# Performance work log

Measured on AMD Instinct MI355X. Metric: run time of the kernel, lower is better.

The kernel has to match this reference:

```python
import jax, jax.numpy as jnp
import numpy as np
from jax import lax

MAXW = 4  # spans cover j in [i, min(i+4, max_len)) -> widths 1..4


def setup_inputs() -> dict:
    key = jax.random.key(0)
    ks = jax.random.split(key, 8)
    B, L, H = 64, 512, 256
    Hd = H // 2  # dynamicLSTM hidden = kernel_num/2
    s = 0.05
    feats = jax.random.normal(ks[0], (B, L, H), dtype=jnp.float32)
    lens = jax.random.randint(ks[1], (B,), 1, L + 1)
    W_ih = jax.random.normal(ks[2], (4 * Hd, H), dtype=jnp.float32) * s
    W_hh = jax.random.normal(ks[3], (4 * Hd, Hd), dtype=jnp.float32) * s
    b_ih = jax.random.normal(ks[4], (4 * Hd,), dtype=jnp.float32) * s
    b_hh = jax.random.normal(ks[5], (4 * Hd,), dtype=jnp.float32) * s
    W_tri = jax.random.normal(ks[6], (2, Hd), dtype=jnp.float32) * s
    b_tri = jax.random.normal(ks[7], (2,), dtype=jnp.float32) * s
    return {"feats": feats, "W_ih": W_ih, "W_hh": W_hh, "b_ih": b_ih,
            "b_hh": b_hh, "W_tri": W_tri, "b_tri": b_tri, "lens": lens}


def _build_tag_graph(feats, W_ih, W_hh, b_ih, b_hh, W_tri, b_tri, lens):
    B, Lmax, H = feats.shape
    Hd = W_hh.shape[1]
    starts = jnp.arange(Lmax)
    idx = starts[:, None] + jnp.arange(MAXW)[None, :]              # (L, 4)
    in_range = idx < Lmax
    win = feats[:, jnp.minimum(idx, Lmax - 1)] * in_range[None, :, :, None]  # (B, L, 4, H)
    x = win.transpose(2, 0, 1, 3).reshape(MAXW, B * Lmax, H)       # steps-major

    def step(carry, xt):
        h, c = carry
        gates = xt @ W_ih.T + b_ih + h @ W_hh.T + b_hh
        i_, f_, g_, o_ = jnp.split(gates, 4, axis=-1)  # torch gate order i,f,g,o
        c = jax.nn.sigmoid(f_) * c + jax.nn.sigmoid(i_) * jnp.tanh(g_)
        h = jax.nn.sigmoid(o_) * jnp.tanh(c)
        return (h, c), h

    h0 = jnp.zeros((B * Lmax, Hd), feats.dtype)
    _, hs = lax.scan(step, (h0, h0), x)                            # (4, B*L, Hd)
    hs = hs.reshape(MAXW, B, Lmax, Hd).transpose(1, 2, 0, 3)       # (B, L, 4, Hd); [...,t,:] = hidden after t+1 steps

    # effective packed length per span: total = clip(lens - i, 0, w); pack uses max(total, 1)
    w = jnp.arange(1, MAXW + 1)                                    # span widths
    rem = lens[:, None] - starts[None, :]                          # (B, L)
    total = jnp.clip(rem[:, :, None], 0, w[None, None, :])         # (B, L, 4)
    Lsel = jnp.maximum(total, 1)
    row_mask = (total > 0).astype(feats.dtype)
    h_span = jnp.take_along_axis(hs, (Lsel - 1)[..., None], axis=2)  # (B, L, 4, Hd)

    emit = (h_span @ W_tri.T + b_tri) * row_mask[..., None]        # (B, L, 4, 2)
    # scatter emit[b, i, w-1] into span_scores[b, i, i+w-1]; drop spans past max_len
    valid_span = in_range  # j = i + (w-1) < Lmax
    emit = emit * valid_span[None, :, :, None]
    j_clamped = jnp.minimum(idx, Lmax - 1)
    span_scores = jnp.zeros((B, Lmax, Lmax, 2), feats.dtype)
    span_scores = span_scores.at[:, starts[:, None], j_clamped].add(emit)
    return span_scores


def reference(feats, W_ih, W_hh, b_ih, b_hh, W_tri, b_tri, lens):
    return _build_tag_graph(feats, W_ih, W_hh, b_ih, b_hh, W_tri, b_tri, lens)
```

## Files before the change

kernel.cpp:

```cpp
#include <hip/hip_runtime.h>
#include <cstddef>

#define NB 64
#define LL 512
#define HH 256
#define HD 128
#define NG 512
#define TI 16

typedef _Float16 half_t;
typedef _Float16 half8 __attribute__((ext_vector_type(8)));
typedef _Float16 half4 __attribute__((ext_vector_type(4)));
typedef float f32x4 __attribute__((ext_vector_type(4)));

#define MFMA16(a, b, c) __builtin_amdgcn_mfma_f32_16x16x32_f16((a), (b), (c), 0, 0, 0)

#define FP 264
#define XP 522
#define HFP 132
#define HBP 136

__device__ __forceinline__ float sigm(float x)  { return 1.0f / (1.0f + __expf(-x)); }
__device__ __forceinline__ float tanhf_(float x){ return 2.0f / (1.0f + __expf(-2.0f * x)) - 1.0f; }

__global__ void prep_weights(const float* __restrict__ Wih, const float* __restrict__ Whh,
                             const float* __restrict__ bih, const float* __restrict__ bhh,
                             half_t* __restrict__ WihH, half_t* __restrict__ WhhH,
                             float* __restrict__ bsum)
{
    const int idx = blockIdx.x * 256 + threadIdx.x;
    if (idx < NG * HH) WihH[idx] = (half_t)Wih[idx];
    if (idx < NG * HD) WhhH[idx] = (half_t)Whh[idx];
    if (idx < NG)      bsum[idx] = bih[idx] + bhh[idx];
}

__global__ __launch_bounds__(256, 2) void span_lstm_mfma(
    const float* __restrict__ feats, const half_t* __restrict__ WihH,
    const half_t* __restrict__ WhhH, const float* __restrict__ bsum,
    const float* __restrict__ W_tri, const float* __restrict__ b_tri,
    const int* __restrict__ lens, float* __restrict__ out)
{
    __shared__ __align__(16) half_t sFeatb[32 * FP];
    __shared__ __align__(16) float  sXG[20 * XP];
    __shared__ __align__(16) float  sHf[16 * HFP];
    __shared__ __align__(16) half_t sHb[16 * HBP];
    __shared__ float sEmit[2][32];

    const int tid = threadIdx.x;
    const int b  = blockIdx.x >> 5;
    const int i0 = (blockIdx.x & 31) * TI;
    const int lens_b = lens[b];

    for (int idx = tid; idx < 20 * 64; idx += 256) {
        const int p  = idx >> 6;
        const int k4 = (idx & 63) << 2;
        const int gp = i0 + p;
        float4 v = make_float4(0.f, 0.f, 0.f, 0.f);
        if (gp < LL) v = *(const float4*)(feats + ((size_t)b * LL + gp) * HH + k4);
        half4 hv = {(half_t)v.x, (half_t)v.y, (half_t)v.z, (half_t)v.w};
        *(half4*)(&sFeatb[p * FP + k4]) = hv;
    }
    __syncthreads();

    const int lane = tid & 63, wv = tid >> 6;
    const int lm = lane & 15;
    const int lq = lane >> 4;

    {
        half8 afr[2][8];
        #pragma unroll
        for (int mt = 0; mt < 2; ++mt)
            #pragma unroll
            for (int kf = 0; kf < 8; ++kf)
                afr[mt][kf] = *(const half8*)(&sFeatb[(16 * mt + lm) * FP + kf * 32 + lq * 8]);

        const int gwv = wv * 128;
        for (int nt = 0; nt < 8; ++nt) {
            const int gb = gwv + nt * 16;
            const float bs = bsum[gb + lm];
            f32x4 acc0 = {0.f, 0.f, 0.f, 0.f}, acc1 = {0.f, 0.f, 0.f, 0.f};
            #pragma unroll
            for (int kf = 0; kf < 8; ++kf) {
                const half8 bfr = *(const half8*)(WihH + (size_t)(gb + lm) * HH + kf * 32 + lq * 8);
                acc0 = MFMA16(afr[0][kf], bfr, acc0);
                acc1 = MFMA16(afr[1][kf], bfr, acc1);
            }
            #pragma unroll
            for (int r = 0; r < 4; ++r)
                sXG[(lq * 4 + r) * XP + gb + lm] = acc0[r] + bs;
            if (lq == 0) {
                #pragma unroll
                for (int r = 0; r < 4; ++r)
                    sXG[(16 + r) * XP + gb + lm] = acc1[r] + bs;
            }
        }
    }

    const int j0 = 32 * wv;
    half8 bf2[2][4][4];
    #pragma unroll
    for (int jt = 0; jt < 2; ++jt)
        #pragma unroll
        for (int ta = 0; ta < 4; ++ta)
            #pragma unroll
            for (int kf = 0; kf < 4; ++kf)
                bf2[jt][ta][kf] = *(const half8*)(WhhH + (size_t)(ta * HD + j0 + jt * 16 + lm) * HD
                                                  + kf * 32 + lq * 8);
    __syncthreads();

    float cc[2][4] = {{0.f, 0.f, 0.f, 0.f}, {0.f, 0.f, 0.f, 0.f}};

    for (int t = 0; t < 4; ++t) {
        float accg[2][4][4];
        if (t > 0) {
            half8 ah[4];
            #pragma unroll
            for (int kf = 0; kf < 4; ++kf)
                ah[kf] = *(const half8*)(&sHb[lm * HBP + kf * 32 + lq * 8]);
            #pragma unroll
            for (int jt = 0; jt < 2; ++jt)
                #pragma unroll
                for (int ta = 0; ta < 4; ++ta) {
                    f32x4 a = {0.f, 0.f, 0.f, 0.f};
                    #pragma unroll
                    for (int kf = 0; kf < 4; ++kf)
                        a = MFMA16(ah[kf], bf2[jt][ta][kf], a);
                    #pragma unroll
                    for (int r = 0; r < 4; ++r) accg[jt][ta][r] = a[r];
                }
        } else {
            #pragma unroll
            for (int jt = 0; jt < 2; ++jt)
                #pragma unroll
                for (int ta = 0; ta < 4; ++ta)
                    #pragma unroll
                    for (int r = 0; r < 4; ++r) accg[jt][ta][r] = 0.f;
        }
        #pragma unroll
        for (int jt = 0; jt < 2; ++jt)
            #pragma unroll
            for (int ta = 0; ta < 4; ++ta)
                #pragma unroll
                for (int r = 0; r < 4; ++r)
                    accg[jt][ta][r] += sXG[(lq * 4 + r + t) * XP + ta * HD + j0 + jt * 16 + lm];

        float hh[2][4];
        #pragma unroll
        for (int jt = 0; jt < 2; ++jt)
            #pragma unroll
            for (int r = 0; r < 4; ++r) {
                const float ig = sigm(accg[jt][0][r]);
                const float fg = sigm(accg[jt][1][r]);
                const float gg = tanhf_(accg[jt][2][r]);
                const float og = sigm(accg[jt][3][r]);
                cc[jt][r] = fg * cc[jt][r] + ig * gg;
                hh[jt][r] = og * tanhf_(cc[jt][r]);
            }
        __syncthreads();
        #pragma unroll
        for (int jt = 0; jt < 2; ++jt)
            #pragma unroll
            for (int r = 0; r < 4; ++r) {
                const int s = lq * 4 + r, j = j0 + jt * 16 + lm;
                sHf[s * HFP + j] = hh[jt][r];
                sHb[s * HBP + j] = (half_t)hh[jt][r];
            }
        __syncthreads();

        if (tid < 128) {
            const int es = tid & 15, etag = (tid >> 4) & 1, ekc = tid >> 5;
            float part = 0.f;
            #pragma unroll
            for (int jj = 0; jj < 8; ++jj) {
                const float4 hv = *(const float4*)(&sHf[es * HFP + ekc * 32 + 4 * jj]);
                const float4 wt = *(const float4*)(W_tri + (size_t)etag * HD + ekc * 32 + 4 * jj);
                part += hv.x * wt.x + hv.y * wt.y + hv.z * wt.z + hv.w * wt.w;
            }
            part += __shfl_down(part, 32);
            if ((tid & 32) == 0) sEmit[tid >> 6][tid & 31] = part;
        }
        __syncthreads();
        if (tid < 32) {
            const int es = tid & 15, etag = tid >> 4;
            const int i = i0 + es;
            const int rem = lens_b - i;
            const int sc = t + 1;
            if (rem > 0 && sc <= rem) {
                const float e = sEmit[0][tid] + sEmit[1][tid] + b_tri[etag];
                const int mm  = rem < 4 ? rem : 4;
                const int whi = (sc >= mm) ? 4 : sc;
                for (int w2 = sc; w2 <= whi; ++w2) {
                    const int jj2 = i + w2 - 1;
                    if (jj2 < LL)
                        out[(((size_t)b * LL + i) * LL + jj2) * 2 + etag] = e;
                }
            }
        }
    }
}

extern "C" void kernel_launch(void* const* d_in, const int* in_sizes, int n_in,
                              void* d_out, int out_size, void* d_ws, size_t ws_size,
                              hipStream_t stream)
{
    const float* feats = (const float*)d_in[0];
    const float* W_ih  = (const float*)d_in[1];
    const float* W_hh  = (const float*)d_in[2];
    const float* b_ih  = (const float*)d_in[3];
    const float* b_hh  = (const float*)d_in[4];
    const float* W_tri = (const float*)d_in[5];
    const float* b_tri = (const float*)d_in[6];
    const int*   lens  = (const int*)d_in[7];
    float* out = (float*)d_out;

    hipMemsetAsync(out, 0, (size_t)out_size * sizeof(float), stream);

    half_t* WihH = (half_t*)d_ws;
    half_t* WhhH = WihH + (size_t)NG * HH;
    float*  bsum = (float*)(WhhH + (size_t)NG * HD);

    prep_weights<<<(NG * HH + 255) / 256, 256, 0, stream>>>(W_ih, W_hh, b_ih, b_hh,
                                                            WihH, WhhH, bsum);
    span_lstm_mfma<<<NB * (LL / TI), 256, 0, stream>>>(feats, WihH, WhhH, bsum,
                                                       W_tri, b_tri, lens, out);
}
```

Before: 292.3 us.

## Fuse output zeroing into LSTM kernel and shrink shared memory with half-precision buffers

Drops the separate memset of the 64x512x512x2 output. Each block now writes its full output rows, zeros included, with float4 stores from a per-block emit table. Gate pre-activations and hidden states are kept in fp16 shared memory, the hidden buffer is double-buffered to remove one barrier per step, and W_hh is streamed from global instead of held in registers. Together these aim to raise occupancy (launch bounds 4), and fast exp2/rcp intrinsics are used for the gates. The cost is lower precision in the gate inputs and more global reads of W_hh each step.

```diff
diff --git a/kernel.cpp b/kernel.cpp
--- a/kernel.cpp
+++ b/kernel.cpp
@@ -15,13 +15,16 @@
 
 #define MFMA16(a, b, c) __builtin_amdgcn_mfma_f32_16x16x32_f16((a), (b), (c), 0, 0, 0)
 
-#define FP 264
-#define XP 522
-#define HFP 132
+#define FP  264
+#define XP2 520
 #define HBP 136
 
-__device__ __forceinline__ float sigm(float x)  { return 1.0f / (1.0f + __expf(-x)); }
-__device__ __forceinline__ float tanhf_(float x){ return 2.0f / (1.0f + __expf(-2.0f * x)) - 1.0f; }
+__device__ __forceinline__ float fsigm(float x) {
+    return __builtin_amdgcn_rcpf(1.0f + __builtin_amdgcn_exp2f(-1.44269504f * x));
+}
+__device__ __forceinline__ float ftanh(float x) {
+    return 2.0f * __builtin_amdgcn_rcpf(1.0f + __builtin_amdgcn_exp2f(-2.88539008f * x)) - 1.0f;
+}
 
 __global__ void prep_weights(const float* __restrict__ Wih, const float* __restrict__ Whh,
                              const float* __restrict__ bih, const float* __restrict__ bhh,
@@ -34,17 +37,16 @@
     if (idx < NG)      bsum[idx] = bih[idx] + bhh[idx];
 }
 
-__global__ __launch_bounds__(256, 2) void span_lstm_mfma(
+__global__ __launch_bounds__(256, 4) void span_lstm_v4(
     const float* __restrict__ feats, const half_t* __restrict__ WihH,
     const half_t* __restrict__ WhhH, const float* __restrict__ bsum,
     const float* __restrict__ W_tri, const float* __restrict__ b_tri,
     const int* __restrict__ lens, float* __restrict__ out)
 {
-    __shared__ __align__(16) half_t sFeatb[32 * FP];
-    __shared__ __align__(16) float  sXG[20 * XP];
-    __shared__ __align__(16) float  sHf[16 * HFP];
-    __shared__ __align__(16) half_t sHb[16 * HBP];
-    __shared__ float sEmit[2][32];
+    __shared__ __align__(16) half_t sFeatb[20 * FP];
+    __shared__ __align__(16) half_t sXGh[20 * XP2];
+    __shared__ __align__(16) half_t sHb[2][16 * HBP];
+    __shared__ float sEmitAll[16][8];
 
     const int tid = threadIdx.x;
     const int b  = blockIdx.x >> 5;
@@ -60,6 +62,7 @@
         half4 hv = {(half_t)v.x, (half_t)v.y, (half_t)v.z, (half_t)v.w};
         *(half4*)(&sFeatb[p * FP + k4]) = hv;
     }
+    if (tid < 128) ((float*)sEmitAll)[tid] = 0.f;
     __syncthreads();
 
     const int lane = tid & 63, wv = tid >> 6;
@@ -67,13 +70,13 @@
     const int lq = lane >> 4;
 
     {
+        const int rowA1 = (16 + lm > 19) ? 19 : 16 + lm;
         half8 afr[2][8];
         #pragma unroll
-        for (int mt = 0; mt < 2; ++mt)
-            #pragma unroll
-            for (int kf = 0; kf < 8; ++kf)
-                afr[mt][kf] = *(const half8*)(&sFeatb[(16 * mt + lm) * FP + kf * 32 + lq * 8]);
-
+        for (int kf = 0; kf < 8; ++kf) {
+            afr[0][kf] = *(const half8*)(&sFeatb[lm * FP + kf * 32 + lq * 8]);
+            afr[1][kf] = *(const half8*)(&sFeatb[rowA1 * FP + kf * 32 + lq * 8]);
+        }
         const int gwv = wv * 128;
         for (int nt = 0; nt < 8; ++nt) {
             const int gb = gwv + nt * 16;
@@ -87,44 +90,38 @@
             }
             #pragma unroll
             for (int r = 0; r < 4; ++r)
-                sXG[(lq * 4 + r) * XP + gb + lm] = acc0[r] + bs;
+                sXGh[(lq * 4 + r) * XP2 + gb + lm] = (half_t)(acc0[r] + bs);
             if (lq == 0) {
                 #pragma unroll
                 for (int r = 0; r < 4; ++r)
-                    sXG[(16 + r) * XP + gb + lm] = acc1[r] + bs;
-            }
-        }
-    }
+                    sXGh[(16 + r) * XP2 + gb + lm] = (half_t)(acc1[r] + bs);
+            }
+        }
+    }
+    __syncthreads();
 
     const int j0 = 32 * wv;
-    half8 bf2[2][4][4];
-    #pragma unroll
-    for (int jt = 0; jt < 2; ++jt)
-        #pragma unroll
-        for (int ta = 0; ta < 4; ++ta)
-            #pragma unroll
-            for (int kf = 0; kf < 4; ++kf)
-                bf2[jt][ta][kf] = *(const half8*)(WhhH + (size_t)(ta * HD + j0 + jt * 16 + lm) * HD
-                                                  + kf * 32 + lq * 8);
-    __syncthreads();
-
     float cc[2][4] = {{0.f, 0.f, 0.f, 0.f}, {0.f, 0.f, 0.f, 0.f}};
 
     for (int t = 0; t < 4; ++t) {
+        const int wb = t & 1, rb = wb ^ 1;
         float accg[2][4][4];
         if (t > 0) {
             half8 ah[4];
             #pragma unroll
             for (int kf = 0; kf < 4; ++kf)
-                ah[kf] = *(const half8*)(&sHb[lm * HBP + kf * 32 + lq * 8]);
+                ah[kf] = *(const half8*)(&sHb[rb][lm * HBP + kf * 32 + lq * 8]);
             #pragma unroll
             for (int jt = 0; jt < 2; ++jt)
                 #pragma unroll
                 for (int ta = 0; ta < 4; ++ta) {
                     f32x4 a = {0.f, 0.f, 0.f, 0.f};
                     #pragma unroll
-                    for (int kf = 0; kf < 4; ++kf)
-                        a = MFMA16(ah[kf], bf2[jt][ta][kf], a);
+                    for (int kf = 0; kf < 4; ++kf) {
+                        const half8 bfr = *(const half8*)(WhhH
+                            + (size_t)(ta * HD + j0 + jt * 16 + lm) * HD + kf * 32 + lq * 8);
+                        a = MFMA16(ah[kf], bfr, a);
+                    }
                     #pragma unroll
                     for (int r = 0; r < 4; ++r) accg[jt][ta][r] = a[r];
                 }
@@ -142,59 +139,65 @@
             for (int ta = 0; ta < 4; ++ta)
                 #pragma unroll
                 for (int r = 0; r < 4; ++r)
-                    accg[jt][ta][r] += sXG[(lq * 4 + r + t) * XP + ta * HD + j0 + jt * 16 + lm];
-
-        float hh[2][4];
+                    accg[jt][ta][r] += (float)sXGh[(lq * 4 + r + t) * XP2 + ta * HD
+                                                   + j0 + jt * 16 + lm];
         #pragma unroll
         for (int jt = 0; jt < 2; ++jt)
             #pragma unroll
             for (int r = 0; r < 4; ++r) {
-                const float ig = sigm(accg[jt][0][r]);
-                const float fg = sigm(accg[jt][1][r]);
-                const float gg = tanhf_(accg[jt][2][r]);
-                const float og = sigm(accg[jt][3][r]);
+                const float ig = fsigm(accg[jt][0][r]);
+                const float fg = fsigm(accg[jt][1][r]);
+                const float gg = ftanh(accg[jt][2][r]);
+                const float og = fsigm(accg[jt][3][r]);
                 cc[jt][r] = fg * cc[jt][r] + ig * gg;
-                hh[jt][r] = og * tanhf_(cc[jt][r]);
+                const float h = og * ftanh(cc[jt][r]);
+                sHb[wb][(lq * 4 + r) * HBP + j0 + jt * 16 + lm] = (half_t)h;
             }
         __syncthreads();
-        #pragma unroll
-        for (int jt = 0; jt < 2; ++jt)
-            #pragma unroll
-            for (int r = 0; r < 4; ++r) {
-                const int s = lq * 4 + r, j = j0 + jt * 16 + lm;
-                sHf[s * HFP + j] = hh[jt][r];
-                sHb[s * HBP + j] = (half_t)hh[jt][r];
-            }
-        __syncthreads();
-
-        if (tid < 128) {
-            const int es = tid & 15, etag = (tid >> 4) & 1, ekc = tid >> 5;
+
+        if (tid < 64) {
+            const int es = tid >> 2, etag = (tid >> 1) & 1, kc = tid & 1;
+            const half_t* hp = &sHb[wb][es * HBP + kc * 64];
+            const float*  wp = W_tri + (size_t)etag * HD + kc * 64;
             float part = 0.f;
             #pragma unroll
-            for (int jj = 0; jj < 8; ++jj) {
-                const float4 hv = *(const float4*)(&sHf[es * HFP + ekc * 32 + 4 * jj]);
-                const float4 wt = *(const float4*)(W_tri + (size_t)etag * HD + ekc * 32 + 4 * jj);
-                part += hv.x * wt.x + hv.y * wt.y + hv.z * wt.z + hv.w * wt.w;
-            }
-            part += __shfl_down(part, 32);
-            if ((tid & 32) == 0) sEmit[tid >> 6][tid & 31] = part;
-        }
-        __syncthreads();
-        if (tid < 32) {
-            const int es = tid & 15, etag = tid >> 4;
-            const int i = i0 + es;
-            const int rem = lens_b - i;
-            const int sc = t + 1;
-            if (rem > 0 && sc <= rem) {
-                const float e = sEmit[0][tid] + sEmit[1][tid] + b_tri[etag];
-                const int mm  = rem < 4 ? rem : 4;
-                const int whi = (sc >= mm) ? 4 : sc;
-                for (int w2 = sc; w2 <= whi; ++w2) {
-                    const int jj2 = i + w2 - 1;
-                    if (jj2 < LL)
-                        out[(((size_t)b * LL + i) * LL + jj2) * 2 + etag] = e;
+            for (int u = 0; u < 64; u += 4) {
+                const half4 h4 = *(const half4*)(hp + u);
+                const float4 w4 = *(const float4*)(wp + u);
+                part += (float)h4.x * w4.x + (float)h4.y * w4.y
+                      + (float)h4.z * w4.z + (float)h4.w * w4.w;
+            }
+            part += __shfl_xor(part, 1);
+            if (kc == 0) {
+                const int i = i0 + es, rem = lens_b - i, sc = t + 1;
+                if (rem > 0 && sc <= rem) {
+                    const float e = part + b_tri[etag];
+                    const int mm  = rem < 4 ? rem : 4;
+                    const int whi = (sc >= mm) ? 4 : sc;
+                    for (int w2 = sc; w2 <= whi; ++w2)
+                        sEmitAll[es][(w2 - 1) * 2 + etag] = e;
                 }
             }
+        }
+    }
+    __syncthreads();
+
+    {
+        const int row = tid >> 4;
+        const int f4b = tid & 15;
+        const int iG  = i0 + row;
+        float* rowp = out + ((size_t)b * LL + iG) * LL * 2;
+        #pragma unroll
+        for (int cth = 0; cth < 16; ++cth) {
+            const int f4 = f4b + 16 * cth;
+            const int c4 = f4 * 4;
+            const int j1 = c4 >> 1;
+            const int d1 = j1 - iG;
+            float4 v = make_float4(0.f, 0.f, 0.f, 0.f);
+            if ((unsigned)d1 < 4u) { v.x = sEmitAll[row][d1 * 2]; v.y = sEmitAll[row][d1 * 2 + 1]; }
+            const int d2 = d1 + 1;
+            if ((unsigned)d2 < 4u) { v.z = sEmitAll[row][d2 * 2]; v.w = sEmitAll[row][d2 * 2 + 1]; }
+            *(float4*)(rowp + c4) = v;
         }
     }
 }
@@ -213,14 +216,12 @@
     const int*   lens  = (const int*)d_in[7];
     float* out = (float*)d_out;
 
-    hipMemsetAsync(out, 0, (size_t)out_size * sizeof(float), stream);
-
     half_t* WihH = (half_t*)d_ws;
     half_t* WhhH = WihH + (size_t)NG * HH;
     float*  bsum = (float*)(WhhH + (size_t)NG * HD);
 
     prep_weights<<<(NG * HH + 255) / 256, 256, 0, stream>>>(W_ih, W_hh, b_ih, b_hh,
                                                             WihH, WhhH, bsum);
-    span_lstm_mfma<<<NB * (LL / TI), 256, 0, stream>>>(feats, WihH, WhhH, bsum,
-                                                       W_tri, b_tri, lens, out);
-}
+    span_lstm_v4<<<NB * (LL / TI), 256, 0, stream>>>(feats, WihH, WhhH, bsum,
+                                                     W_tri, b_tri, lens, out);
+}
```

After: 333.5 us. +14.1%, slower.
